# Kernel optimization log

Hardware: AMD Instinct MI355X
Metric: run time of the kernel (lower is better)

## Reference

```python
import jax, jax.numpy as jnp
import numpy as np

B, L, D, H = 2, 256, 128, 256


def silu_bwd(x):
    # NOTE: replicates the module's silu_backward exactly: silu(x) + sigmoid(x)*(1 - silu(x))
    s = jax.nn.silu(x)
    return s + jax.nn.sigmoid(x) * (1.0 - s)


def setup_inputs() -> dict:
    key = jax.random.key(0)
    ks = jax.random.split(key, 10)
    f32 = jnp.float32
    return {
        "x": jax.random.normal(ks[0], (B, L, D), f32),
        "W1_init": jax.random.normal(ks[1], (H, D), f32) * H ** -0.5,
        "b1_init": jnp.zeros((H,), f32),
        "W2_init": jax.random.normal(ks[2], (D, H), f32) * D ** -0.5,
        "b2_init": jnp.zeros((D,), f32),
        "Wq": jax.random.normal(ks[3], (D, D), f32) * D ** -0.5,
        "bq": jnp.zeros((D,), f32),
        "Wk": jax.random.normal(ks[4], (D, D), f32) * D ** -0.5,
        "bk": jnp.zeros((D,), f32),
        "Wv": jax.random.normal(ks[5], (D, D), f32) * D ** -0.5,
        "bv": jnp.zeros((D,), f32),
        "Wlr": jax.random.normal(ks[6], (1, D), f32) * D ** -0.5,
        "blr": jnp.zeros((1,), f32),
        "Wm": jax.random.normal(ks[7], (1, D), f32) * D ** -0.5,
        "bm": jnp.zeros((1,), f32),
        "Wwd": jax.random.normal(ks[8], (1, D), f32) * D ** -0.5,
        "bwd": jnp.zeros((1,), f32),
    }


def _forward(x, W1_init, b1_init, W2_init, b2_init, Wq, bq, Wk, bk, Wv, bv,
             Wlr, blr, Wm, bm, Wwd, bwd):
    b, l, d = x.shape
    q = x @ Wq.T + bq
    k = x @ Wk.T + bk
    v = x @ Wv.T + bv

    # fast-weight forward pass with initial weights (first call: state = init params)
    Z1 = jnp.einsum('hd,bld->blh', W1_init, k) + b1_init
    X2 = jax.nn.silu(Z1)
    Z2 = jnp.einsum('dh,blh->bld', W2_init, X2) + b2_init

    # per-token gradients of 0.5*||Z2 - v||^2
    gZ2 = Z2 - v
    gW2 = jnp.einsum('bld,blh->bldh', gZ2, X2)
    gX2 = jnp.einsum('bld,dh->blh', gZ2, W2_init)
    gZ1 = gX2 * silu_bwd(Z1)
    gW1 = jnp.einsum('blh,bld->blhd', gZ1, k)

    lr = jax.nn.softplus(x @ Wlr.T + blr)[..., 0]  # (b,l)
    gW1 = gW1 * lr[:, :, None, None]
    gb1 = gZ1 * lr[:, :, None]
    gW2 = gW2 * lr[:, :, None, None]
    gb2 = gZ2 * lr[:, :, None]

    strict = jnp.tril(jnp.ones((l, l), x.dtype), -1)  # row > col
    incl = jnp.tril(jnp.ones((l, l), x.dtype))        # row >= col

    # momentum: masked log-cumsum trick; [b,l,m] decay matrix
    log_mom = -jax.nn.softplus(-(x @ Wm.T + bm))[..., 0]  # (b,l)
    mom_cs = jnp.exp(jnp.cumsum(log_mom[:, :, None] * strict, axis=1)) * incl
    mW1 = jnp.einsum('blm,bmhd->blhd', mom_cs, gW1)
    mb1 = jnp.einsum('blm,bmh->blh', mom_cs, gb1)
    mW2 = jnp.einsum('blm,bmdh->bldh', mom_cs, gW2)
    mb2 = jnp.einsum('blm,bmd->bld', mom_cs, gb2)
    # cross-chunk momentum terms vanish (momentum state initialized to zero)

    # weight decay gating
    log_wd = -jax.nn.softplus(-(x @ Wwd.T + bwd))[..., 0]
    wd_cs = jnp.exp(jnp.cumsum(log_wd[:, :, None] * strict, axis=1)) * incl
    wd_full = jnp.exp(jnp.cumsum(log_wd, axis=1))  # (b,l)

    W1p = jnp.einsum('blm,bmhd->blhd', wd_cs, mW1) + wd_full[:, :, None, None] * W1_init
    b1p = jnp.einsum('blm,bmh->blh', wd_cs, mb1) + wd_full[:, :, None] * b1_init
    W2p = jnp.einsum('blm,bmdh->bldh', wd_cs, mW2) + wd_full[:, :, None, None] * W2_init
    b2p = jnp.einsum('blm,bmd->bld', wd_cs, mb2) + wd_full[:, :, None] * b2_init

    # query the per-token updated fast weights
    Zq1 = jnp.einsum('blhd,bld->blh', W1p, q) + b1p
    Xq2 = jax.nn.silu(Zq1)
    Zq2 = jnp.einsum('bldh,blh->bld', W2p, Xq2) + b2p
    return Zq2


def reference(x, W1_init, b1_init, W2_init, b2_init, Wq, bq, Wk, bk, Wv, bv,
              Wlr, blr, Wm, bm, Wwd, bwd):
    return _forward(x, W1_init, b1_init, W2_init, b2_init, Wq, bq, Wk, bk, Wv, bv,
                    Wlr, blr, Wm, bm, Wwd, bwd)
```

## Files before the change

### kernel.cpp

```cpp
#include <hip/hip_runtime.h>
#include <hip/hip_bf16.h>


#define Bc 2
#define Lc 256
#define Dc 128
#define Hc 256

__device__ __forceinline__ float sigf(float z)  { return 1.f / (1.f + expf(-z)); }
__device__ __forceinline__ float siluf(float z) { return z * sigf(z); }
__device__ __forceinline__ float silubwdf(float z) {
    float sg = sigf(z);
    float s  = z * sg;
    return s + sg * (1.f - s);
}
__device__ __forceinline__ float softplusf(float z) {
    if (z > 20.f)  return z;
    if (z < -20.f) return expf(z);
    return log1pf(expf(z));
}
__device__ __forceinline__ float dot4(float4 a, float4 b) {
    return a.x*b.x + a.y*b.y + a.z*b.z + a.w*b.w;
}

__global__ __launch_bounds__(256) void k_pre(
    const float* __restrict__ Wq, const float* __restrict__ Wk,
    const float* __restrict__ Wv, const float* __restrict__ W1,
    const float* __restrict__ W2,
    float4* __restrict__ Wq4, float4* __restrict__ Wk4, float4* __restrict__ Wv4,
    float4* __restrict__ W14, float4* __restrict__ W2q4, float4* __restrict__ W2c4,
    const float* __restrict__ x,
    const float* __restrict__ Wlr, const float* __restrict__ blr,
    const float* __restrict__ Wm,  const float* __restrict__ bm,
    const float* __restrict__ Wwd, const float* __restrict__ bwd,
    float* __restrict__ Ssc, float* __restrict__ wdf)
{
    const int bb = blockIdx.x;
    if (bb < 144) {
        if (bb < 112) {
            const float* in; float4* o; int M, N, base;
            if      (bb < 16) { in = Wq; o = Wq4;  M = 128; N = 128; base = 0;  }
            else if (bb < 32) { in = Wk; o = Wk4;  M = 128; N = 128; base = 16; }
            else if (bb < 48) { in = Wv; o = Wv4;  M = 128; N = 128; base = 32; }
            else if (bb < 80) { in = W1; o = W14;  M = 256; N = 128; base = 48; }
            else              { in = W2; o = W2q4; M = 128; N = 256; base = 80; }
            const int idx = (bb - base) * 256 + threadIdx.x;
            const int r = idx % M, g = idx / M;
            o[idx] = *(const float4*)(in + r * N + 4 * g);
        } else {
            const int idx = (bb - 112) * 256 + threadIdx.x;
            const int c = idx & 255, g = idx >> 8;
            W2c4[idx] = make_float4(W2[(4*g+0)*Hc + c], W2[(4*g+1)*Hc + c],
                                    W2[(4*g+2)*Hc + c], W2[(4*g+3)*Hc + c]);
        }
        return;
    }

    __shared__ float lrS[Lc], lwS[Lc], ewdS[Lc], clmS[Lc], cwdS[Lc];
    const int b = bb - 144;
    const int l = threadIdx.x;

    const float4* xr4 = (const float4*)(x + (b * Lc + l) * Dc);
    const float4* wl4 = (const float4*)Wlr;
    const float4* wm4 = (const float4*)Wm;
    const float4* ww4 = (const float4*)Wwd;
    float dlr = blr[0], dm = bm[0], dw = bwd[0];
    #pragma unroll 4
    for (int j = 0; j < Dc / 4; ++j) {
        float4 xv = xr4[j];
        dlr += dot4(wl4[j], xv);
        dm  += dot4(wm4[j], xv);
        dw  += dot4(ww4[j], xv);
    }
    lrS[l] = softplusf(dlr);
    float lm = -softplusf(-dm);
    float lw = -softplusf(-dw);
    lwS[l]  = lw;
    clmS[l] = lm;
    cwdS[l] = lw;
    __syncthreads();

    for (int off = 1; off < Lc; off <<= 1) {
        float a = (l >= off) ? clmS[l - off] : 0.f;
        float c = (l >= off) ? cwdS[l - off] : 0.f;
        __syncthreads();
        clmS[l] += a; cwdS[l] += c;
        __syncthreads();
    }
    wdf[b * Lc + l] = expf(cwdS[l]);
    ewdS[l] = __expf(lwS[l]);
    __syncthreads();

    const int   m     = l;
    const float clm_m = clmS[m];
    const float lrm   = lrS[m];
    float* outp = Ssc + (b * Lc) * Lc + m;
    float s = 0.f;
    for (int ll = 0; ll < Lc; ++ll) {
        float e2 = __expf(clmS[ll] - clm_m);
        s = (ll >= m) ? (ewdS[ll] * s + e2) : 0.f;
        outp[ll * Lc] = s * lrm;
    }
}

__global__ __launch_bounds__(512, 4) void k_token(
    const float* __restrict__ x,
    const float* __restrict__ b1v, const float* __restrict__ b2v,
    const float* __restrict__ bq,  const float* __restrict__ bk,
    const float* __restrict__ bv,
    const float4* __restrict__ Wq4, const float4* __restrict__ Wk4,
    const float4* __restrict__ Wv4, const float4* __restrict__ W14,
    const float4* __restrict__ W2q4, const float4* __restrict__ W2c4,
    float* __restrict__ qo, float* __restrict__ KT, float* __restrict__ X2T,
    float* __restrict__ z1q, float* __restrict__ GZ1, float* __restrict__ GZ2)
{
    __shared__ __align__(16) float xs[Dc], qs[Dc], ks[Dc];
    __shared__ __align__(16) float X2s[Hc], z1s[Hc], gZ2s[Dc];
    __shared__ __align__(16) float pv[2][Dc], pz[4][Dc], pg[2][Hc];

    const int t0  = blockIdx.x;
    const int b   = t0 >> 8;
    const int l0  = t0 & 255;
    const int tid = threadIdx.x;

    if (tid < Dc / 4)
        ((float4*)xs)[tid] = ((const float4*)(x + t0 * Dc))[tid];
    __syncthreads();

    {
        const int g = tid >> 7, c = tid & 127;
        float4 wb[8];
        if (g < 2) {
            const float4* W = g ? Wk4 : Wq4;
            float a = (g ? bk : bq)[c];
            for (int j4 = 0; j4 < 32; j4 += 8) {
                #pragma unroll
                for (int u = 0; u < 8; ++u) wb[u] = W[(j4+u) * Dc + c];
                #pragma unroll
                for (int u = 0; u < 8; ++u)
                    a += dot4(wb[u], *(const float4*)&xs[4*(j4+u)]);
            }
            if (g == 0) {
                qs[c] = a;
                qo[t0 * Dc + c] = a;
            } else {
                ks[c] = a;
                KT[(size_t)b * 32768 + ((c >> 2) * Lc + l0) * 4 + (c & 3)] = a;
            }
        } else {
            const int half = g - 2;
            const int j0 = half * 16;
            float av = 0.f;
            for (int j4 = j0; j4 < j0 + 16; j4 += 8) {
                #pragma unroll
                for (int u = 0; u < 8; ++u) wb[u] = Wv4[(j4+u) * Dc + c];
                #pragma unroll
                for (int u = 0; u < 8; ++u)
                    av += dot4(wb[u], *(const float4*)&xs[4*(j4+u)]);
            }
            pv[half][c] = av;
        }
    }
    __syncthreads();

    {
        const int which = tid >> 8, h = tid & 255;
        const float* src = which ? qs : ks;
        float a = b1v[h];
        float4 wb[8];
        for (int d4 = 0; d4 < 32; d4 += 8) {
            #pragma unroll
            for (int u = 0; u < 8; ++u) wb[u] = W14[(d4+u) * Hc + h];
            #pragma unroll
            for (int u = 0; u < 8; ++u)
                a += dot4(wb[u], *(const float4*)&src[4*(d4+u)]);
        }
        if (which == 0) {
            z1s[h] = a;
            float s = siluf(a);
            X2s[h] = s;
            X2T[(size_t)b * 65536 + ((h >> 2) * Lc + l0) * 4 + (h & 3)] = s;
        } else {
            z1q[t0 * Hc + h] = a;
        }
    }
    __syncthreads();

    {
        const int q4g = tid >> 7, d = tid & 127;
        const int h0 = q4g * 16;
        float a = 0.f;
        float4 wb[8];
        for (int h4 = h0; h4 < h0 + 16; h4 += 8) {
            #pragma unroll
            for (int u = 0; u < 8; ++u) wb[u] = W2q4[(h4+u) * Dc + d];
            #pragma unroll
            for (int u = 0; u < 8; ++u)
                a += dot4(wb[u], *(const float4*)&X2s[4*(h4+u)]);
        }
        pz[q4g][d] = a;
    }
    __syncthreads();
    if (tid < Dc) {
        const int d = tid;
        float g = pz[0][d] + pz[1][d] + pz[2][d] + pz[3][d] + b2v[d]
                - (pv[0][d] + pv[1][d] + bv[d]);
        gZ2s[d] = g;
        GZ2[(size_t)b * 32768 + ((l0 >> 2) * Dc + d) * 4 + (l0 & 3)] = g;
    }
    __syncthreads();

    {
        const int which = tid >> 8, h = tid & 255;
        const int d0 = which * 16;
        float a = 0.f;
        float4 wb[8];
        for (int d4 = d0; d4 < d0 + 16; d4 += 8) {
            #pragma unroll
            for (int u = 0; u < 8; ++u) wb[u] = W2c4[(d4+u) * Hc + h];
            #pragma unroll
            for (int u = 0; u < 8; ++u)
                a += dot4(wb[u], *(const float4*)&gZ2s[4*(d4+u)]);
        }
        pg[which][h] = a;
    }
    __syncthreads();
    if (tid < Hc) {
        const int h = tid;
        GZ1[(size_t)b * 65536 + ((l0 >> 2) * Hc + h) * 4 + (l0 & 3)]
            = (pg[0][h] + pg[1][h]) * silubwdf(z1s[h]);
    }
}

__global__ __launch_bounds__(512, 4) void k_query(
    const float* __restrict__ qo,  const float* __restrict__ KT,
    const float* __restrict__ X2T, const float* __restrict__ GZ1,
    const float* __restrict__ GZ2, const float* __restrict__ z1q,
    const float* __restrict__ Ssc, const float* __restrict__ wdf,
    const float4* __restrict__ W2q4, const float* __restrict__ b2v,
    float* __restrict__ out)
{
    __shared__ __align__(16) float qs[Dc], ss[Lc], arow[Lc], xq2s[Hc];
    __shared__ __align__(16) float ps[2][Lc], pq[2][Hc], pm[4][Dc], pw[4][Dc];

    const int t0  = blockIdx.x;
    const int b   = t0 >> 8;
    const int l0  = t0 & 255;
    const int tid = threadIdx.x;
    const int M4  = (l0 >> 2) + 1;
    const int mPad = M4 * 4;

    if (tid < Dc / 4)
        ((float4*)qs)[tid] = ((const float4*)(qo + t0 * Dc))[tid];
    if (tid < Lc) ss[tid] = Ssc[t0 * Lc + tid];
    const float wdf_t = wdf[t0];
    __syncthreads();

    {
        const int which = tid >> 8, m = tid & 255;
        if (m < mPad) {
            const float4* ktb = (const float4*)(KT + (size_t)b * 32768);
            const int d0 = which * 16;
            float acc = 0.f;
            float4 wb[8];
            for (int d4 = d0; d4 < d0 + 16; d4 += 8) {
                #pragma unroll
                for (int u = 0; u < 8; ++u) wb[u] = ktb[(d4+u) * Lc + m];
                #pragma unroll
                for (int u = 0; u < 8; ++u)
                    acc += dot4(wb[u], *(const float4*)&qs[4*(d4+u)]);
            }
            ps[which][m] = acc;
        }
    }
    __syncthreads();
    if (tid < mPad) arow[tid] = ss[tid] * (ps[0][tid] + ps[1][tid] + 1.f);
    __syncthreads();

    {
        const int which = tid >> 8, h = tid & 255;
        const float4* g = (const float4*)(GZ1 + (size_t)b * 65536);
        const float4* ar4 = (const float4*)arow;
        float acc = 0.f;
        float4 wb[8];
        int m4 = which;
        for (; m4 + 14 < M4; m4 += 16) {
            #pragma unroll
            for (int u = 0; u < 8; ++u) wb[u] = g[(m4 + 2*u) * Hc + h];
            #pragma unroll
            for (int u = 0; u < 8; ++u) acc += dot4(wb[u], ar4[m4 + 2*u]);
        }
        for (; m4 < M4; m4 += 2) acc += dot4(g[m4 * Hc + h], ar4[m4]);
        pq[which][h] = acc;
    }
    __syncthreads();
    if (tid < Hc)
        xq2s[tid] = siluf(pq[0][tid] + pq[1][tid] + wdf_t * z1q[t0 * Hc + tid]);
    __syncthreads();

    {
        const int which = tid >> 8, m = tid & 255;
        if (m < mPad) {
            const float4* xtb = (const float4*)(X2T + (size_t)b * 65536);
            const int h0 = which * 32;
            float acc = 0.f;
            float4 wb[8];
            for (int h4 = h0; h4 < h0 + 32; h4 += 8) {
                #pragma unroll
                for (int u = 0; u < 8; ++u) wb[u] = xtb[(h4+u) * Lc + m];
                #pragma unroll
                for (int u = 0; u < 8; ++u)
                    acc += dot4(wb[u], *(const float4*)&xq2s[4*(h4+u)]);
            }
            ps[which][m] = acc;
        }
    }
    __syncthreads();
    if (tid < mPad) arow[tid] = ss[tid] * (ps[0][tid] + ps[1][tid] + 1.f);
    __syncthreads();

    {
        const int q4g = tid >> 7, d = tid & 127;
        const float4* g2  = (const float4*)(GZ2 + (size_t)b * 32768);
        const float4* ar4 = (const float4*)arow;
        float am = 0.f, aw = 0.f;
        float4 wb[8];
        int m4 = q4g;
        for (; m4 + 28 < M4; m4 += 32) {
            #pragma unroll
            for (int u = 0; u < 8; ++u) wb[u] = g2[(m4 + 4*u) * Dc + d];
            #pragma unroll
            for (int u = 0; u < 8; ++u) am += dot4(wb[u], ar4[m4 + 4*u]);
        }
        for (; m4 < M4; m4 += 4) am += dot4(g2[m4 * Dc + d], ar4[m4]);
        const int h0 = q4g * 16;
        for (int h4 = h0; h4 < h0 + 16; h4 += 8) {
            #pragma unroll
            for (int u = 0; u < 8; ++u) wb[u] = W2q4[(h4+u) * Dc + d];
            #pragma unroll
            for (int u = 0; u < 8; ++u)
                aw += dot4(wb[u], *(const float4*)&xq2s[4*(h4+u)]);
        }
        pm[q4g][d] = am; pw[q4g][d] = aw;
    }
    __syncthreads();
    if (tid < Dc) {
        const int d = tid;
        out[t0 * Dc + d] = (pm[0][d] + pm[1][d] + pm[2][d] + pm[3][d])
            + wdf_t * (b2v[d] + pw[0][d] + pw[1][d] + pw[2][d] + pw[3][d]);
    }
}

extern "C" void kernel_launch(void* const* d_in, const int* in_sizes, int n_in,
                              void* d_out, int out_size, void* d_ws, size_t ws_size,
                              hipStream_t stream)
{
    const float* x   = (const float*)d_in[0];
    const float* W1  = (const float*)d_in[1];
    const float* b1  = (const float*)d_in[2];
    const float* W2  = (const float*)d_in[3];
    const float* b2  = (const float*)d_in[4];
    const float* Wq  = (const float*)d_in[5];
    const float* bq  = (const float*)d_in[6];
    const float* Wk  = (const float*)d_in[7];
    const float* bk  = (const float*)d_in[8];
    const float* Wv  = (const float*)d_in[9];
    const float* bv  = (const float*)d_in[10];
    const float* Wlr = (const float*)d_in[11];
    const float* blr = (const float*)d_in[12];
    const float* Wm  = (const float*)d_in[13];
    const float* bm  = (const float*)d_in[14];
    const float* Wwd = (const float*)d_in[15];
    const float* bwd = (const float*)d_in[16];

    float* ws = (float*)d_ws;
    float*  qo   = ws;
    float*  KT   = ws + 65536;
    float*  X2T  = ws + 131072;
    float*  GZ1  = ws + 262144;
    float*  GZ2  = ws + 393216;
    float*  z1q  = ws + 458752;
    float*  Ssc  = ws + 589824;
    float*  wdf  = ws + 720896;
    float4* Wq4  = (float4*)(ws + 721408);
    float4* Wk4  = (float4*)(ws + 737792);
    float4* Wv4  = (float4*)(ws + 754176);
    float4* W14  = (float4*)(ws + 770560);
    float4* W2q4 = (float4*)(ws + 803328);
    float4* W2c4 = (float4*)(ws + 836096);
    float*  out  = (float*)d_out;

    k_pre<<<146, 256, 0, stream>>>(Wq, Wk, Wv, W1, W2,
                                   Wq4, Wk4, Wv4, W14, W2q4, W2c4,
                                   x, Wlr, blr, Wm, bm, Wwd, bwd, Ssc, wdf);
    k_token<<<Bc * Lc, 512, 0, stream>>>(x, b1, b2, bq, bk, bv,
                                         Wq4, Wk4, Wv4, W14, W2q4, W2c4,
                                         qo, KT, X2T, z1q, GZ1, GZ2);
    k_query<<<Bc * Lc, 512, 0, stream>>>(qo, KT, X2T, GZ1, GZ2, z1q,
                                         Ssc, wdf, W2q4, b2, out);
}
```

Measured before the change: 146.2 us.

## Process two tokens per block to reuse weight and state loads

Result: faster. 139.2 us (-4.8%).

```diff
diff --git a/kernel.cpp b/kernel.cpp
--- a/kernel.cpp
+++ b/kernel.cpp
@@ -114,17 +114,17 @@
     float* __restrict__ qo, float* __restrict__ KT, float* __restrict__ X2T,
     float* __restrict__ z1q, float* __restrict__ GZ1, float* __restrict__ GZ2)
 {
-    __shared__ __align__(16) float xs[Dc], qs[Dc], ks[Dc];
-    __shared__ __align__(16) float X2s[Hc], z1s[Hc], gZ2s[Dc];
-    __shared__ __align__(16) float pv[2][Dc], pz[4][Dc], pg[2][Hc];
-
-    const int t0  = blockIdx.x;
+    __shared__ __align__(16) float xs[2][Dc], qs[2][Dc], ks[2][Dc];
+    __shared__ __align__(16) float X2s[2][Hc], z1s[2][Hc], gZ2s[2][Dc];
+    __shared__ __align__(16) float pv[2][2][Dc], pz[4][2][Dc], pg[2][2][Hc];
+
+    const int t0  = blockIdx.x * 2;
     const int b   = t0 >> 8;
     const int l0  = t0 & 255;
     const int tid = threadIdx.x;
 
-    if (tid < Dc / 4)
-        ((float4*)xs)[tid] = ((const float4*)(x + t0 * Dc))[tid];
+    if (tid < 2 * Dc / 4)
+        ((float4*)&xs[0][0])[tid] = ((const float4*)(x + t0 * Dc))[tid];
     __syncthreads();
 
     {
@@ -132,56 +132,67 @@
         float4 wb[8];
         if (g < 2) {
             const float4* W = g ? Wk4 : Wq4;
-            float a = (g ? bk : bq)[c];
+            float a0 = (g ? bk : bq)[c], a1 = a0;
             for (int j4 = 0; j4 < 32; j4 += 8) {
                 #pragma unroll
                 for (int u = 0; u < 8; ++u) wb[u] = W[(j4+u) * Dc + c];
                 #pragma unroll
-                for (int u = 0; u < 8; ++u)
-                    a += dot4(wb[u], *(const float4*)&xs[4*(j4+u)]);
+                for (int u = 0; u < 8; ++u) {
+                    a0 += dot4(wb[u], *(const float4*)&xs[0][4*(j4+u)]);
+                    a1 += dot4(wb[u], *(const float4*)&xs[1][4*(j4+u)]);
+                }
             }
             if (g == 0) {
-                qs[c] = a;
-                qo[t0 * Dc + c] = a;
+                qs[0][c] = a0; qs[1][c] = a1;
+                qo[t0 * Dc + c] = a0;
+                qo[(t0 + 1) * Dc + c] = a1;
             } else {
-                ks[c] = a;
-                KT[(size_t)b * 32768 + ((c >> 2) * Lc + l0) * 4 + (c & 3)] = a;
+                ks[0][c] = a0; ks[1][c] = a1;
+                float* ktp = KT + (size_t)b * 32768;
+                ktp[((c >> 2) * Lc + l0 + 0) * 4 + (c & 3)] = a0;
+                ktp[((c >> 2) * Lc + l0 + 1) * 4 + (c & 3)] = a1;
             }
         } else {
-            const int half = g - 2;
-            const int j0 = half * 16;
-            float av = 0.f;
+            const int half = g - 2, j0 = half * 16;
+            float av0 = 0.f, av1 = 0.f;
             for (int j4 = j0; j4 < j0 + 16; j4 += 8) {
                 #pragma unroll
                 for (int u = 0; u < 8; ++u) wb[u] = Wv4[(j4+u) * Dc + c];
                 #pragma unroll
-                for (int u = 0; u < 8; ++u)
-                    av += dot4(wb[u], *(const float4*)&xs[4*(j4+u)]);
-            }
-            pv[half][c] = av;
+                for (int u = 0; u < 8; ++u) {
+                    av0 += dot4(wb[u], *(const float4*)&xs[0][4*(j4+u)]);
+                    av1 += dot4(wb[u], *(const float4*)&xs[1][4*(j4+u)]);
+                }
+            }
+            pv[half][0][c] = av0; pv[half][1][c] = av1;
         }
     }
     __syncthreads();
 
     {
         const int which = tid >> 8, h = tid & 255;
-        const float* src = which ? qs : ks;
-        float a = b1v[h];
+        const float (*src)[Dc] = which ? qs : ks;
+        float a0 = b1v[h], a1 = a0;
         float4 wb[8];
         for (int d4 = 0; d4 < 32; d4 += 8) {
             #pragma unroll
             for (int u = 0; u < 8; ++u) wb[u] = W14[(d4+u) * Hc + h];
             #pragma unroll
-            for (int u = 0; u < 8; ++u)
-                a += dot4(wb[u], *(const float4*)&src[4*(d4+u)]);
+            for (int u = 0; u < 8; ++u) {
+                a0 += dot4(wb[u], *(const float4*)&src[0][4*(d4+u)]);
+                a1 += dot4(wb[u], *(const float4*)&src[1][4*(d4+u)]);
+            }
         }
         if (which == 0) {
-            z1s[h] = a;
-            float s = siluf(a);
-            X2s[h] = s;
-            X2T[(size_t)b * 65536 + ((h >> 2) * Lc + l0) * 4 + (h & 3)] = s;
+            z1s[0][h] = a0; z1s[1][h] = a1;
+            float s0 = siluf(a0), s1 = siluf(a1);
+            X2s[0][h] = s0; X2s[1][h] = s1;
+            float* xtp = X2T + (size_t)b * 65536;
+            xtp[((h >> 2) * Lc + l0 + 0) * 4 + (h & 3)] = s0;
+            xtp[((h >> 2) * Lc + l0 + 1) * 4 + (h & 3)] = s1;
         } else {
-            z1q[t0 * Hc + h] = a;
+            z1q[(t0 + 0) * Hc + h] = a0;
+            z1q[(t0 + 1) * Hc + h] = a1;
         }
     }
     __syncthreads();
@@ -189,46 +200,52 @@
     {
         const int q4g = tid >> 7, d = tid & 127;
         const int h0 = q4g * 16;
-        float a = 0.f;
+        float a0 = 0.f, a1 = 0.f;
         float4 wb[8];
         for (int h4 = h0; h4 < h0 + 16; h4 += 8) {
             #pragma unroll
             for (int u = 0; u < 8; ++u) wb[u] = W2q4[(h4+u) * Dc + d];
             #pragma unroll
-            for (int u = 0; u < 8; ++u)
-                a += dot4(wb[u], *(const float4*)&X2s[4*(h4+u)]);
-        }
-        pz[q4g][d] = a;
-    }
-    __syncthreads();
-    if (tid < Dc) {
-        const int d = tid;
-        float g = pz[0][d] + pz[1][d] + pz[2][d] + pz[3][d] + b2v[d]
-                - (pv[0][d] + pv[1][d] + bv[d]);
-        gZ2s[d] = g;
-        GZ2[(size_t)b * 32768 + ((l0 >> 2) * Dc + d) * 4 + (l0 & 3)] = g;
+            for (int u = 0; u < 8; ++u) {
+                a0 += dot4(wb[u], *(const float4*)&X2s[0][4*(h4+u)]);
+                a1 += dot4(wb[u], *(const float4*)&X2s[1][4*(h4+u)]);
+            }
+        }
+        pz[q4g][0][d] = a0; pz[q4g][1][d] = a1;
+    }
+    __syncthreads();
+    if (tid < 2 * Dc) {
+        const int t = tid >> 7, d = tid & 127;
+        float g = pz[0][t][d] + pz[1][t][d] + pz[2][t][d] + pz[3][t][d] + b2v[d]
+                - (pv[0][t][d] + pv[1][t][d] + bv[d]);
+        gZ2s[t][d] = g;
+        const int l = l0 + t;
+        GZ2[(size_t)b * 32768 + ((l >> 2) * Dc + d) * 4 + (l & 3)] = g;
     }
     __syncthreads();
 
     {
         const int which = tid >> 8, h = tid & 255;
         const int d0 = which * 16;
-        float a = 0.f;
+        float a0 = 0.f, a1 = 0.f;
         float4 wb[8];
         for (int d4 = d0; d4 < d0 + 16; d4 += 8) {
             #pragma unroll
             for (int u = 0; u < 8; ++u) wb[u] = W2c4[(d4+u) * Hc + h];
             #pragma unroll
-            for (int u = 0; u < 8; ++u)
-                a += dot4(wb[u], *(const float4*)&gZ2s[4*(d4+u)]);
-        }
-        pg[which][h] = a;
-    }
-    __syncthreads();
-    if (tid < Hc) {
-        const int h = tid;
-        GZ1[(size_t)b * 65536 + ((l0 >> 2) * Hc + h) * 4 + (l0 & 3)]
-            = (pg[0][h] + pg[1][h]) * silubwdf(z1s[h]);
+            for (int u = 0; u < 8; ++u) {
+                a0 += dot4(wb[u], *(const float4*)&gZ2s[0][4*(d4+u)]);
+                a1 += dot4(wb[u], *(const float4*)&gZ2s[1][4*(d4+u)]);
+            }
+        }
+        pg[which][0][h] = a0; pg[which][1][h] = a1;
+    }
+    __syncthreads();
+    {
+        const int t = tid >> 8, h = tid & 255;
+        const int l = l0 + t;
+        GZ1[(size_t)b * 65536 + ((l >> 2) * Hc + h) * 4 + (l & 3)]
+            = (pg[0][t][h] + pg[1][t][h]) * silubwdf(z1s[t][h]);
     }
 }
 
@@ -240,20 +257,24 @@
     const float4* __restrict__ W2q4, const float* __restrict__ b2v,
     float* __restrict__ out)
 {
-    __shared__ __align__(16) float qs[Dc], ss[Lc], arow[Lc], xq2s[Hc];
-    __shared__ __align__(16) float ps[2][Lc], pq[2][Hc], pm[4][Dc], pw[4][Dc];
-
-    const int t0  = blockIdx.x;
+    __shared__ __align__(16) float qs[2][Dc], ss[2][Lc], arow[2][Lc], xq2s[2][Hc];
+    __shared__ __align__(16) float ps[2][2][Lc], pq[2][2][Hc];
+    __shared__ __align__(16) float pm[4][2][Dc], pw[4][2][Dc];
+
+    const int t0  = blockIdx.x * 2;
     const int b   = t0 >> 8;
     const int l0  = t0 & 255;
     const int tid = threadIdx.x;
-    const int M4  = (l0 >> 2) + 1;
+    const int M4  = ((l0 + 1) >> 2) + 1;
     const int mPad = M4 * 4;
 
-    if (tid < Dc / 4)
-        ((float4*)qs)[tid] = ((const float4*)(qo + t0 * Dc))[tid];
-    if (tid < Lc) ss[tid] = Ssc[t0 * Lc + tid];
-    const float wdf_t = wdf[t0];
+    if (tid < 2 * Dc / 4)
+        ((float4*)&qs[0][0])[tid] = ((const float4*)(qo + t0 * Dc))[tid];
+    if (tid < Lc) {
+        ss[0][tid] = Ssc[(t0 + 0) * Lc + tid];
+        ss[1][tid] = Ssc[(t0 + 1) * Lc + tid];
+    }
+    const float wdf0 = wdf[t0 + 0], wdf1 = wdf[t0 + 1];
     __syncthreads();
 
     {
@@ -261,41 +282,59 @@
         if (m < mPad) {
             const float4* ktb = (const float4*)(KT + (size_t)b * 32768);
             const int d0 = which * 16;
-            float acc = 0.f;
+            float acc0 = 0.f, acc1 = 0.f;
             float4 wb[8];
             for (int d4 = d0; d4 < d0 + 16; d4 += 8) {
                 #pragma unroll
                 for (int u = 0; u < 8; ++u) wb[u] = ktb[(d4+u) * Lc + m];
                 #pragma unroll
-                for (int u = 0; u < 8; ++u)
-                    acc += dot4(wb[u], *(const float4*)&qs[4*(d4+u)]);
-            }
-            ps[which][m] = acc;
-        }
-    }
-    __syncthreads();
-    if (tid < mPad) arow[tid] = ss[tid] * (ps[0][tid] + ps[1][tid] + 1.f);
+                for (int u = 0; u < 8; ++u) {
+                    acc0 += dot4(wb[u], *(const float4*)&qs[0][4*(d4+u)]);
+                    acc1 += dot4(wb[u], *(const float4*)&qs[1][4*(d4+u)]);
+                }
+            }
+            ps[which][0][m] = acc0; ps[which][1][m] = acc1;
+        }
+    }
+    __syncthreads();
+    {
+        const int t = tid >> 8, m = tid & 255;
+        if (m < mPad)
+            arow[t][m] = ss[t][m] * (ps[0][t][m] + ps[1][t][m] + 1.f);
+    }
     __syncthreads();
 
     {
         const int which = tid >> 8, h = tid & 255;
         const float4* g = (const float4*)(GZ1 + (size_t)b * 65536);
-        const float4* ar4 = (const float4*)arow;
-        float acc = 0.f;
+        const float4* ar0 = (const float4*)&arow[0][0];
+        const float4* ar1 = (const float4*)&arow[1][0];
+        float acc0 = 0.f, acc1 = 0.f;
         float4 wb[8];
         int m4 = which;
         for (; m4 + 14 < M4; m4 += 16) {
             #pragma unroll
             for (int u = 0; u < 8; ++u) wb[u] = g[(m4 + 2*u) * Hc + h];
             #pragma unroll
-            for (int u = 0; u < 8; ++u) acc += dot4(wb[u], ar4[m4 + 2*u]);
-        }
-        for (; m4 < M4; m4 += 2) acc += dot4(g[m4 * Hc + h], ar4[m4]);
-        pq[which][h] = acc;
-    }
-    __syncthreads();
-    if (tid < Hc)
-        xq2s[tid] = siluf(pq[0][tid] + pq[1][tid] + wdf_t * z1q[t0 * Hc + tid]);
+            for (int u = 0; u < 8; ++u) {
+                acc0 += dot4(wb[u], ar0[m4 + 2*u]);
+                acc1 += dot4(wb[u], ar1[m4 + 2*u]);
+            }
+        }
+        for (; m4 < M4; m4 += 2) {
+            float4 gv = g[m4 * Hc + h];
+            acc0 += dot4(gv, ar0[m4]);
+            acc1 += dot4(gv, ar1[m4]);
+        }
+        pq[which][0][h] = acc0; pq[which][1][h] = acc1;
+    }
+    __syncthreads();
+    {
+        const int t = tid >> 8, h = tid & 255;
+        const float w = t ? wdf1 : wdf0;
+        xq2s[t][h] = siluf(pq[0][t][h] + pq[1][t][h]
+                           + w * z1q[(t0 + t) * Hc + h]);
+    }
     __syncthreads();
 
     {
@@ -303,51 +342,70 @@
         if (m < mPad) {
             const float4* xtb = (const float4*)(X2T + (size_t)b * 65536);
             const int h0 = which * 32;
-            float acc = 0.f;
+            float acc0 = 0.f, acc1 = 0.f;
             float4 wb[8];
             for (int h4 = h0; h4 < h0 + 32; h4 += 8) {
                 #pragma unroll
                 for (int u = 0; u < 8; ++u) wb[u] = xtb[(h4+u) * Lc + m];
                 #pragma unroll
-                for (int u = 0; u < 8; ++u)
-                    acc += dot4(wb[u], *(const float4*)&xq2s[4*(h4+u)]);
-            }
-            ps[which][m] = acc;
-        }
-    }
-    __syncthreads();
-    if (tid < mPad) arow[tid] = ss[tid] * (ps[0][tid] + ps[1][tid] + 1.f);
+                for (int u = 0; u < 8; ++u) {
+                    acc0 += dot4(wb[u], *(const float4*)&xq2s[0][4*(h4+u)]);
+                    acc1 += dot4(wb[u], *(const float4*)&xq2s[1][4*(h4+u)]);
+                }
+            }
+            ps[which][0][m] = acc0; ps[which][1][m] = acc1;
+        }
+    }
+    __syncthreads();
+    {
+        const int t = tid >> 8, m = tid & 255;
+        if (m < mPad)
+            arow[t][m] = ss[t][m] * (ps[0][t][m] + ps[1][t][m] + 1.f);
+    }
     __syncthreads();
 
     {
         const int q4g = tid >> 7, d = tid & 127;
         const float4* g2  = (const float4*)(GZ2 + (size_t)b * 32768);
-        const float4* ar4 = (const float4*)arow;
-        float am = 0.f, aw = 0.f;
+        const float4* ar0 = (const float4*)&arow[0][0];
+        const float4* ar1 = (const float4*)&arow[1][0];
+        float am0 = 0.f, am1 = 0.f, aw0 = 0.f, aw1 = 0.f;
         float4 wb[8];
         int m4 = q4g;
         for (; m4 + 28 < M4; m4 += 32) {
             #pragma unroll
             for (int u = 0; u < 8; ++u) wb[u] = g2[(m4 + 4*u) * Dc + d];
             #pragma unroll
-            for (int u = 0; u < 8; ++u) am += dot4(wb[u], ar4[m4 + 4*u]);
-        }
-        for (; m4 < M4; m4 += 4) am += dot4(g2[m4 * Dc + d], ar4[m4]);
+            for (int u = 0; u < 8; ++u) {
+                am0 += dot4(wb[u], ar0[m4 + 4*u]);
+                am1 += dot4(wb[u], ar1[m4 + 4*u]);
+            }
+        }
+        for (; m4 < M4; m4 += 4) {
+            float4 gv = g2[m4 * Dc + d];
+            am0 += dot4(gv, ar0[m4]);
+            am1 += dot4(gv, ar1[m4]);
+        }
         const int h0 = q4g * 16;
         for (int h4 = h0; h4 < h0 + 16; h4 += 8) {
             #pragma unroll
             for (int u = 0; u < 8; ++u) wb[u] = W2q4[(h4+u) * Dc + d];
             #pragma unroll
-            for (int u = 0; u < 8; ++u)
-                aw += dot4(wb[u], *(const float4*)&xq2s[4*(h4+u)]);
-        }
-        pm[q4g][d] = am; pw[q4g][d] = aw;
-    }
-    __syncthreads();
-    if (tid < Dc) {
-        const int d = tid;
-        out[t0 * Dc + d] = (pm[0][d] + pm[1][d] + pm[2][d] + pm[3][d])
-            + wdf_t * (b2v[d] + pw[0][d] + pw[1][d] + pw[2][d] + pw[3][d]);
+            for (int u = 0; u < 8; ++u) {
+                aw0 += dot4(wb[u], *(const float4*)&xq2s[0][4*(h4+u)]);
+                aw1 += dot4(wb[u], *(const float4*)&xq2s[1][4*(h4+u)]);
+            }
+        }
+        pm[q4g][0][d] = am0; pm[q4g][1][d] = am1;
+        pw[q4g][0][d] = aw0; pw[q4g][1][d] = aw1;
+    }
+    __syncthreads();
+    if (tid < 2 * Dc) {
+        const int t = tid >> 7, d = tid & 127;
+        const float w = t ? wdf1 : wdf0;
+        out[(t0 + t) * Dc + d] =
+            (pm[0][t][d] + pm[1][t][d] + pm[2][t][d] + pm[3][t][d])
+            + w * (b2v[d] + pw[0][t][d] + pw[1][t][d] + pw[2][t][d] + pw[3][t][d]);
     }
 }
 
@@ -393,9 +451,9 @@
     k_pre<<<146, 256, 0, stream>>>(Wq, Wk, Wv, W1, W2,
                                    Wq4, Wk4, Wv4, W14, W2q4, W2c4,
                                    x, Wlr, blr, Wm, bm, Wwd, bwd, Ssc, wdf);
-    k_token<<<Bc * Lc, 512, 0, stream>>>(x, b1, b2, bq, bk, bv,
-                                         Wq4, Wk4, Wv4, W14, W2q4, W2c4,
-                                         qo, KT, X2T, z1q, GZ1, GZ2);
-    k_query<<<Bc * Lc, 512, 0, stream>>>(qo, KT, X2T, GZ1, GZ2, z1q,
-                                         Ssc, wdf, W2q4, b2, out);
-}
+    k_token<<<Bc * Lc / 2, 512, 0, stream>>>(x, b1, b2, bq, bk, bv,
+                                             Wq4, Wk4, Wv4, W14, W2q4, W2c4,
+                                             qo, KT, X2T, z1q, GZ1, GZ2);
+    k_query<<<Bc * Lc / 2, 512, 0, stream>>>(qo, KT, X2T, GZ1, GZ2, z1q,
+                                             Ssc, wdf, W2q4, b2, out);
+}
```
